# Kernel tuning notes

Measured on AMD Instinct MI355X. Metric: run time of the kernel, lower is better.

The kernel has to match this reference:

```python
import jax, jax.numpy as jnp
import numpy as np

N = 262144
FEAT = 64
D = 128
DEPTH = 2
N_LAYERS = 1
SCALE_FEATURES = 0.5
SCALE_STEPS = (1.0 - SCALE_FEATURES) / DEPTH
LN_EPS = 1e-5
SLOPE = 0.01


def leaky(x):
    return jnp.where(x >= 0, x, SLOPE * x)


def layernorm(x):
    mu = x.mean(-1, keepdims=True)
    var = ((x - mu) ** 2).mean(-1, keepdims=True)
    return (x - mu) / jnp.sqrt(var + LN_EPS)


def setup_inputs() -> dict:
    key = jax.random.key(0)
    ks = jax.random.split(key, 12)
    raw_feats = jax.random.normal(ks[0], (N, FEAT), dtype=jnp.float32)
    uids = jnp.arange(N, dtype=jnp.int32)
    id_map = jax.random.randint(ks[1], (N, 1, 2), 0, N, dtype=jnp.int32)
    # FeatureEmbedder params
    slow_mean = jnp.zeros((FEAT,), jnp.float32)
    slow_std = jnp.ones((FEAT,), jnp.float32)
    W_embd = jax.random.normal(ks[2], (FEAT, D), jnp.float32) / np.sqrt(FEAT)
    b_embd = jnp.zeros((D,), jnp.float32)
    Wl = jax.random.normal(ks[3], (N_LAYERS, D, D), jnp.float32) / np.sqrt(D)
    bl = jnp.zeros((N_LAYERS, D), jnp.float32)
    # node_emb params
    W_node = jax.random.normal(ks[4], (D, D), jnp.float32) / np.sqrt(D)
    b_node = jnp.zeros((D,), jnp.float32)
    rezero = jnp.full((1,), 0.1, jnp.float32)  # nonzero so depth loop is active
    W_w = jax.random.normal(ks[5], (D, 1), jnp.float32) * 0.01
    W_v = jax.random.normal(ks[6], (D, 1), jnp.float32) / np.sqrt(D)
    return {
        'raw_feats': raw_feats, 'uids': uids, 'id_map': id_map,
        'slow_mean': slow_mean, 'slow_std': slow_std,
        'W_embd': W_embd, 'b_embd': b_embd, 'Wl': Wl, 'bl': bl,
        'W_node': W_node, 'b_node': b_node, 'rezero': rezero,
        'W_w': W_w, 'W_v': W_v,
    }


def reference(raw_feats, uids, id_map, slow_mean, slow_std, W_embd, b_embd,
              Wl, bl, W_node, b_node, rezero, W_w, W_v):
    # sorted_feats = cat([raw_feats, zeros(1, FEAT)])  -> [N+1, FEAT]
    sorted_feats = jnp.concatenate(
        [raw_feats, jnp.zeros((1, FEAT), raw_feats.dtype)], axis=0)

    # FeatureEmbedder: SlowNorm -> Linear -> leaky, residual blocks, LayerNorm, *scale
    x = (sorted_feats - slow_mean) / (slow_std + 0.001)
    x = leaky(x @ W_embd + b_embd)
    for i in range(N_LAYERS):
        # F.leaky_relu(Sequential(Linear, LeakyReLU)(x)) + x  (double leaky)
        x = leaky(leaky(x @ Wl[i] + bl[i])) + x
    x = layernorm(x) * SCALE_FEATURES  # [N+1, D]

    # uids == arange(N), so uid-value -> row-index lookup is identity
    ids = id_map[:, 0, :]  # [N, 2] row indices into x

    for _ in range(DEPTH):
        feats = x[ids].mean(axis=1)                 # gather [N,2,D] -> mean -> [N,D]
        feats = leaky(feats @ W_node + b_node)       # node_emb
        new = x[:-1] + feats * (SCALE_STEPS * rezero)
        x = jnp.concatenate([new, x[-1:]], axis=0)   # scatter-update rows [:-1]

    x_main = x[:-1]
    w = x_main @ W_w                                  # weight head, no bias
    v = jax.lax.stop_gradient(x_main) @ W_v           # value head on detached x
    return (x_main, w, v)
```

## Files before the change

kernel.cpp:

```cpp
#include <hip/hip_runtime.h>


#define NROWS 262144
#define NBLK  4096

typedef __attribute__((ext_vector_type(8))) short bhalf8;
typedef __attribute__((ext_vector_type(4))) float f32x4;
typedef __attribute__((ext_vector_type(4))) unsigned int u32x4;

__device__ __forceinline__ unsigned short f2bf(float x) {
    union { float f; unsigned u; } v; v.f = x;
    unsigned r = v.u + 0x7FFFu + ((v.u >> 16) & 1u);
    return (unsigned short)(r >> 16);
}
__device__ __forceinline__ float bflo(unsigned u) {
    union { unsigned u; float f; } v; v.u = u << 16; return v.f;
}
__device__ __forceinline__ float bfhi(unsigned u) {
    union { unsigned u; float f; } v; v.u = u & 0xFFFF0000u; return v.f;
}
__device__ __forceinline__ float bf2f(unsigned short s) {
    union { unsigned u; float f; } v; v.u = ((unsigned)s) << 16; return v.f;
}
__device__ __forceinline__ float leaky(float x) { return x >= 0.0f ? x : 0.01f * x; }

__global__ void __launch_bounds__(256)
setup_kernel(const float* __restrict__ smean, const float* __restrict__ sstd,
             const float* __restrict__ Wemb, const float* __restrict__ bemb,
             const float* __restrict__ Wl, const float* __restrict__ Wn,
             unsigned short* __restrict__ wpack, float* __restrict__ bembP)
{
    int task = blockIdx.x * 256 + threadIdx.x;
    if (blockIdx.x < 160) {
        if (task < 8192) {
            int f = task >> 9, idx = task & 511;
            int t = f >> 1, s = f & 1, lane = idx >> 3, j = idx & 7;
            int n = t * 16 + (lane & 15), k = s * 32 + (lane >> 4) * 8 + j;
            wpack[task] = f2bf(Wemb[k * 128 + n] / (sstd[k] + 0.001f));
        } else if (task < 24576) {
            int u = task - 8192;
            int f = u >> 9, idx = u & 511;
            int t = f >> 2, s = f & 3, lane = idx >> 3, j = idx & 7;
            int n = t * 16 + (lane & 15), k = s * 32 + (lane >> 4) * 8 + j;
            wpack[task] = f2bf(Wl[k * 128 + n]);
        } else if (task < 40960) {
            int u = task - 24576;
            int f = u >> 9, idx = u & 511;
            int t = f >> 2, s = f & 3, lane = idx >> 3, j = idx & 7;
            int n = t * 16 + (lane & 15), k = s * 32 + (lane >> 4) * 8 + j;
            wpack[task] = f2bf(0.5f * Wn[k * 128 + n]);
        }
    } else {
        int n = threadIdx.x;
        if (n < 128) {
            float acc = bemb[n];
            for (int k = 0; k < 64; k++)
                acc -= smean[k] / (sstd[k] + 0.001f) * Wemb[k * 128 + n];
            bembP[n] = acc;
        }
    }
}

__global__ void __launch_bounds__(256, 6)
phase_a_kernel(const float* __restrict__ feats,
               const unsigned short* __restrict__ wembF,
               const float* __restrict__ bembP,
               const unsigned short* __restrict__ wlF,
               const float* __restrict__ bl,
               unsigned short* __restrict__ xout)
{
    __shared__ __align__(16) short hb[64 * 136];
    const int tid = threadIdx.x, lane = tid & 63, wv = tid >> 6;
    const int m = lane & 15, q = lane >> 4;
    const int crow = tid >> 4, ccb = tid & 15;
    const int r0 = blockIdx.x * 64;

    const bhalf8* wbe = (const bhalf8*)wembF;
    const bhalf8* wbl = (const bhalf8*)wlF;

    bhalf8 af[2];
    #pragma unroll
    for (int s = 0; s < 2; s++) {
        const float* fp = feats + (size_t)(r0 + wv * 16 + m) * 64 + s * 32 + q * 8;
        f32x4 f0 = *(const f32x4*)fp;
        f32x4 f1 = *(const f32x4*)(fp + 4);
        bhalf8 a;
        #pragma unroll
        for (int jj = 0; jj < 4; jj++) { a[jj] = (short)f2bf(f0[jj]); a[4 + jj] = (short)f2bf(f1[jj]); }
        af[s] = a;
    }
    f32x4 acc[8] = {};
    #pragma unroll
    for (int s = 0; s < 2; s++)
        #pragma unroll
        for (int t = 0; t < 8; t++)
            acc[t] = __builtin_amdgcn_mfma_f32_16x16x32_bf16(af[s], wbe[(t * 2 + s) * 64 + lane], acc[t], 0, 0, 0);

    #pragma unroll
    for (int t = 0; t < 8; t++) {
        float be = bembP[t * 16 + m];
        #pragma unroll
        for (int p = 0; p < 4; p++)
            hb[(wv * 16 + q * 4 + p) * 136 + t * 16 + m] = (short)f2bf(leaky(acc[t][p] + be));
    }
    f32x4 acc2[8] = {};
    #pragma unroll
    for (int s = 0; s < 4; s++) {
        bhalf8 a = *(const bhalf8*)&hb[(wv * 16 + m) * 136 + s * 32 + q * 8];
        #pragma unroll
        for (int t = 0; t < 8; t++)
            acc2[t] = __builtin_amdgcn_mfma_f32_16x16x32_bf16(a, wbl[(t * 4 + s) * 64 + lane], acc2[t], 0, 0, 0);
    }

    float sum[4] = {0, 0, 0, 0}, ssq[4] = {0, 0, 0, 0};
    #pragma unroll
    for (int t = 0; t < 8; t++) {
        float bb = bl[t * 16 + m];
        #pragma unroll
        for (int p = 0; p < 4; p++) {
            float h = bf2f((unsigned short)hb[(wv * 16 + q * 4 + p) * 136 + t * 16 + m]);
            float v = leaky(leaky(acc2[t][p] + bb)) + h;
            acc2[t][p] = v;
            sum[p] += v; ssq[p] += v * v;
        }
    }
    #pragma unroll
    for (int p = 0; p < 4; p++) {
        #pragma unroll
        for (int d = 1; d < 16; d <<= 1) {
            sum[p] += __shfl_xor(sum[p], d, 64);
            ssq[p] += __shfl_xor(ssq[p], d, 64);
        }
    }
    #pragma unroll
    for (int p = 0; p < 4; p++) {
        float mu  = sum[p] * (1.0f / 128.0f);
        float var = ssq[p] * (1.0f / 128.0f) - mu * mu;
        float rs  = rsqrtf(var + 1e-5f) * 0.5f;
        int row = wv * 16 + q * 4 + p;
        #pragma unroll
        for (int t = 0; t < 8; t++)
            hb[row * 136 + t * 16 + m] = (short)f2bf((acc2[t][p] - mu) * rs);
    }
    __syncthreads();
    #pragma unroll
    for (int i = 0; i < 4; i++) {
        int row = i * 16 + crow;
        *reinterpret_cast<u32x4*>(&xout[(size_t)(r0 + row) * 128 + ccb * 8]) =
            *reinterpret_cast<const u32x4*>(&hb[row * 136 + ccb * 8]);
    }
}

template <typename TOUT>
__global__ void __launch_bounds__(256, 6)
prop_kernel(const unsigned short* __restrict__ xin, const int* __restrict__ idmap,
            const unsigned short* __restrict__ wnF, const float* __restrict__ bn,
            const float* __restrict__ rez, const float* __restrict__ Ww,
            const float* __restrict__ Wv, TOUT* __restrict__ xout,
            float* __restrict__ wout, float* __restrict__ vout, int final_pass)
{
    __shared__ __align__(16) short gls[64 * 136];
    const int tid = threadIdx.x, lane = tid & 63, wv = tid >> 6;
    const int m = lane & 15, q = lane >> 4;
    const int crow = tid >> 4, ccb = tid & 15;
    const int r0 = blockIdx.x * 64;
    const bhalf8* wbn = (const bhalf8*)wnF;
    const float scale = 0.25f * rez[0];

    const int myrow = r0 + wv * 16 + m;
    int2 ids = ((const int2*)idmap)[myrow];
    const unsigned short* xa = xin + (size_t)ids.x * 128 + q * 8;
    const unsigned short* xb = xin + (size_t)ids.y * 128 + q * 8;
    u32x4 ga[4], gb[4];
    #pragma unroll
    for (int s = 0; s < 4; s++) {
        ga[s] = *(const u32x4*)(xa + s * 32);
        gb[s] = *(const u32x4*)(xb + s * 32);
    }

    f32x4 acc[8] = {};
    #pragma unroll
    for (int s = 0; s < 4; s++) {
        bhalf8 a;
        #pragma unroll
        for (int w = 0; w < 4; w++) {
            a[2 * w]     = (short)f2bf(bflo(ga[s][w]) + bflo(gb[s][w]));
            a[2 * w + 1] = (short)f2bf(bfhi(ga[s][w]) + bfhi(gb[s][w]));
        }
        #pragma unroll
        for (int t = 0; t < 8; t++)
            acc[t] = __builtin_amdgcn_mfma_f32_16x16x32_bf16(a, wbn[(t * 4 + s) * 64 + lane], acc[t], 0, 0, 0);
    }

    #pragma unroll
    for (int t = 0; t < 8; t++) {
        float bb = bn[t * 16 + m];
        #pragma unroll
        for (int p = 0; p < 4; p++)
            gls[(wv * 16 + q * 4 + p) * 136 + t * 16 + m] = (short)f2bf(leaky(acc[t][p] + bb) * scale);
    }
    __syncthreads();

    #pragma unroll
    for (int i = 0; i < 4; i++) {
        int row = i * 16 + crow;
        u32x4 gv = *(const u32x4*)&gls[row * 136 + ccb * 8];
        u32x4 xv = *(const u32x4*)(xin + (size_t)(r0 + row) * 128 + ccb * 8);
        float xn[8];
        #pragma unroll
        for (int w = 0; w < 4; w++) {
            xn[2 * w]     = bflo(xv[w]) + bflo(gv[w]);
            xn[2 * w + 1] = bfhi(xv[w]) + bfhi(gv[w]);
        }
        if (!final_pass) {
            u32x4 ov;
            #pragma unroll
            for (int w = 0; w < 4; w++)
                ov[w] = (unsigned)f2bf(xn[2 * w]) | ((unsigned)f2bf(xn[2 * w + 1]) << 16);
            *reinterpret_cast<u32x4*>(reinterpret_cast<unsigned short*>(xout) + (size_t)(r0 + row) * 128 + ccb * 8) = ov;
        } else {
            float* op = reinterpret_cast<float*>(xout) + (size_t)(r0 + row) * 128 + ccb * 8;
            f32x4 o0, o1;
            #pragma unroll
            for (int w = 0; w < 4; w++) { o0[w] = xn[w]; o1[w] = xn[4 + w]; }
            __builtin_nontemporal_store(o0, reinterpret_cast<f32x4*>(op));
            __builtin_nontemporal_store(o1, reinterpret_cast<f32x4*>(op + 4));
            f32x4 w0 = *(const f32x4*)&Ww[ccb * 8], w1 = *(const f32x4*)&Ww[ccb * 8 + 4];
            f32x4 v0 = *(const f32x4*)&Wv[ccb * 8], v1 = *(const f32x4*)&Wv[ccb * 8 + 4];
            float ws = 0.0f, vs = 0.0f;
            #pragma unroll
            for (int w = 0; w < 4; w++) {
                ws += xn[w] * w0[w] + xn[4 + w] * w1[w];
                vs += xn[w] * v0[w] + xn[4 + w] * v1[w];
            }
            #pragma unroll
            for (int d = 1; d < 16; d <<= 1) {
                ws += __shfl_xor(ws, d, 64);
                vs += __shfl_xor(vs, d, 64);
            }
            if ((lane & 15) == 0) { wout[r0 + row] = ws; vout[r0 + row] = vs; }
        }
    }
}

extern "C" void kernel_launch(void* const* d_in, const int* in_sizes, int n_in,
                              void* d_out, int out_size, void* d_ws, size_t ws_size,
                              hipStream_t stream) {
    const float* feats = (const float*)d_in[0];
    const int*   idmap = (const int*)d_in[2];
    const float* smean = (const float*)d_in[3];
    const float* sstd  = (const float*)d_in[4];
    const float* Wemb  = (const float*)d_in[5];
    const float* bemb  = (const float*)d_in[6];
    const float* Wl    = (const float*)d_in[7];
    const float* bl    = (const float*)d_in[8];
    const float* Wn    = (const float*)d_in[9];
    const float* bn    = (const float*)d_in[10];
    const float* rez   = (const float*)d_in[11];
    const float* Ww    = (const float*)d_in[12];
    const float* Wv    = (const float*)d_in[13];

    char* ws = (char*)d_ws;
    unsigned short* wpack = (unsigned short*)ws;
    float*          bembP = (float*)(ws + 81920);
    unsigned short* x1    = (unsigned short*)(ws + (1ull << 20));

    float* out = (float*)d_out;
    unsigned short* x0 = (unsigned short*)d_out;
    float* wout = out + (size_t)NROWS * 128;
    float* vout = wout + NROWS;

    setup_kernel<<<161, 256, 0, stream>>>(smean, sstd, Wemb, bemb, Wl, Wn, wpack, bembP);
    phase_a_kernel<<<NBLK, 256, 0, stream>>>(feats, wpack, bembP, wpack + 8192, bl, x0);
    prop_kernel<unsigned short><<<NBLK, 256, 0, stream>>>(x0, idmap, wpack + 24576, bn, rez, Ww, Wv,
                                                          x1, nullptr, nullptr, 0);
    prop_kernel<float><<<NBLK, 256, 0, stream>>>(x1, idmap, wpack + 24576, bn, rez, Ww, Wv,
                                                 out, wout, vout, 1);
}
```

Baseline: 378.1 us.

## Tune cache hints, launch bounds, and keep residual in registers

Several unrelated tweaks land together. Phase A keeps the packed bf16 residual in registers instead of re-reading it from LDS, converts the output copy into a strided loop, and lowers its launch-bounds occupancy hint from 6 to 4. Gather and input loads become nontemporal, which risks poor reuse of gathered rows that are shared across nodes. The final fp32 stores drop their nontemporal hint, and the prop kernel loses its min-blocks hint, which may change register allocation.

```diff
diff --git a/kernel.cpp b/kernel.cpp
--- a/kernel.cpp
+++ b/kernel.cpp
@@ -18,9 +18,6 @@
 }
 __device__ __forceinline__ float bfhi(unsigned u) {
     union { unsigned u; float f; } v; v.u = u & 0xFFFF0000u; return v.f;
-}
-__device__ __forceinline__ float bf2f(unsigned short s) {
-    union { unsigned u; float f; } v; v.u = ((unsigned)s) << 16; return v.f;
 }
 __device__ __forceinline__ float leaky(float x) { return x >= 0.0f ? x : 0.01f * x; }
 
@@ -61,7 +58,7 @@
     }
 }
 
-__global__ void __launch_bounds__(256, 6)
+__global__ void __launch_bounds__(256, 4)
 phase_a_kernel(const float* __restrict__ feats,
                const unsigned short* __restrict__ wembF,
                const float* __restrict__ bembP,
@@ -72,7 +69,6 @@
     __shared__ __align__(16) short hb[64 * 136];
     const int tid = threadIdx.x, lane = tid & 63, wv = tid >> 6;
     const int m = lane & 15, q = lane >> 4;
-    const int crow = tid >> 4, ccb = tid & 15;
     const int r0 = blockIdx.x * 64;
 
     const bhalf8* wbe = (const bhalf8*)wembF;
@@ -82,8 +78,8 @@
     #pragma unroll
     for (int s = 0; s < 2; s++) {
         const float* fp = feats + (size_t)(r0 + wv * 16 + m) * 64 + s * 32 + q * 8;
-        f32x4 f0 = *(const f32x4*)fp;
-        f32x4 f1 = *(const f32x4*)(fp + 4);
+        f32x4 f0 = __builtin_nontemporal_load((const f32x4*)fp);
+        f32x4 f1 = __builtin_nontemporal_load((const f32x4*)(fp + 4));
         bhalf8 a;
         #pragma unroll
         for (int jj = 0; jj < 4; jj++) { a[jj] = (short)f2bf(f0[jj]); a[4 + jj] = (short)f2bf(f1[jj]); }
@@ -96,12 +92,19 @@
         for (int t = 0; t < 8; t++)
             acc[t] = __builtin_amdgcn_mfma_f32_16x16x32_bf16(af[s], wbe[(t * 2 + s) * 64 + lane], acc[t], 0, 0, 0);
 
+    unsigned hvp[8][2];
     #pragma unroll
     for (int t = 0; t < 8; t++) {
         float be = bembP[t * 16 + m];
-        #pragma unroll
-        for (int p = 0; p < 4; p++)
-            hb[(wv * 16 + q * 4 + p) * 136 + t * 16 + m] = (short)f2bf(leaky(acc[t][p] + be));
+        unsigned short hq[4];
+        #pragma unroll
+        for (int p = 0; p < 4; p++) {
+            float h = leaky(acc[t][p] + be);
+            hq[p] = f2bf(h);
+            hb[(wv * 16 + q * 4 + p) * 136 + t * 16 + m] = (short)hq[p];
+        }
+        hvp[t][0] = (unsigned)hq[0] | ((unsigned)hq[1] << 16);
+        hvp[t][1] = (unsigned)hq[2] | ((unsigned)hq[3] << 16);
     }
     f32x4 acc2[8] = {};
     #pragma unroll
@@ -116,10 +119,12 @@
     #pragma unroll
     for (int t = 0; t < 8; t++) {
         float bb = bl[t * 16 + m];
+        float h0 = bflo(hvp[t][0]), h1 = bfhi(hvp[t][0]);
+        float h2 = bflo(hvp[t][1]), h3 = bfhi(hvp[t][1]);
+        float hvv[4] = { h0, h1, h2, h3 };
         #pragma unroll
         for (int p = 0; p < 4; p++) {
-            float h = bf2f((unsigned short)hb[(wv * 16 + q * 4 + p) * 136 + t * 16 + m]);
-            float v = leaky(leaky(acc2[t][p] + bb)) + h;
+            float v = leaky(leaky(acc2[t][p] + bb)) + hvv[p];
             acc2[t][p] = v;
             sum[p] += v; ssq[p] += v * v;
         }
@@ -143,16 +148,15 @@
             hb[row * 136 + t * 16 + m] = (short)f2bf((acc2[t][p] - mu) * rs);
     }
     __syncthreads();
-    #pragma unroll
-    for (int i = 0; i < 4; i++) {
-        int row = i * 16 + crow;
-        *reinterpret_cast<u32x4*>(&xout[(size_t)(r0 + row) * 128 + ccb * 8]) =
-            *reinterpret_cast<const u32x4*>(&hb[row * 136 + ccb * 8]);
+    for (int c = tid; c < 64 * 16; c += 256) {
+        int row = c >> 4, cb = (c & 15) * 8;
+        *reinterpret_cast<u32x4*>(&xout[(size_t)(r0 + row) * 128 + cb]) =
+            *reinterpret_cast<const u32x4*>(&hb[row * 136 + cb]);
     }
 }
 
 template <typename TOUT>
-__global__ void __launch_bounds__(256, 6)
+__global__ void __launch_bounds__(256)
 prop_kernel(const unsigned short* __restrict__ xin, const int* __restrict__ idmap,
             const unsigned short* __restrict__ wnF, const float* __restrict__ bn,
             const float* __restrict__ rez, const float* __restrict__ Ww,
@@ -174,8 +178,8 @@
     u32x4 ga[4], gb[4];
     #pragma unroll
     for (int s = 0; s < 4; s++) {
-        ga[s] = *(const u32x4*)(xa + s * 32);
-        gb[s] = *(const u32x4*)(xb + s * 32);
+        ga[s] = __builtin_nontemporal_load((const u32x4*)(xa + s * 32));
+        gb[s] = __builtin_nontemporal_load((const u32x4*)(xb + s * 32));
     }
 
     f32x4 acc[8] = {};
@@ -205,7 +209,8 @@
     for (int i = 0; i < 4; i++) {
         int row = i * 16 + crow;
         u32x4 gv = *(const u32x4*)&gls[row * 136 + ccb * 8];
-        u32x4 xv = *(const u32x4*)(xin + (size_t)(r0 + row) * 128 + ccb * 8);
+        u32x4 xv = __builtin_nontemporal_load(
+            (const u32x4*)(xin + (size_t)(r0 + row) * 128 + ccb * 8));
         float xn[8];
         #pragma unroll
         for (int w = 0; w < 4; w++) {
@@ -223,8 +228,8 @@
             f32x4 o0, o1;
             #pragma unroll
             for (int w = 0; w < 4; w++) { o0[w] = xn[w]; o1[w] = xn[4 + w]; }
-            __builtin_nontemporal_store(o0, reinterpret_cast<f32x4*>(op));
-            __builtin_nontemporal_store(o1, reinterpret_cast<f32x4*>(op + 4));
+            *reinterpret_cast<f32x4*>(op)     = o0;
+            *reinterpret_cast<f32x4*>(op + 4) = o1;
             f32x4 w0 = *(const f32x4*)&Ww[ccb * 8], w1 = *(const f32x4*)&Ww[ccb * 8 + 4];
             f32x4 v0 = *(const f32x4*)&Wv[ccb * 8], v1 = *(const f32x4*)&Wv[ccb * 8 + 4];
             float ws = 0.0f, vs = 0.0f;
```

Result: slower. 399.4 us (+5.6%).
